# Kernel tuning notes

Measured on AMD Instinct MI355X. Metric: run time of the kernel, lower is better.

Reference implementation:

```python
import jax, jax.numpy as jnp
import numpy as np

B, T, I, H = 64, 512, 1024, 1024


def setup_inputs() -> dict:
    key = jax.random.key(0)
    k1, k2, k3, k4 = jax.random.split(key, 4)
    stdv = 1.0 / np.sqrt(H)
    x = jax.random.normal(k1, (B, T, I), dtype=jnp.float32)
    w_ih = jax.random.uniform(k2, (4 * H, I), minval=-stdv, maxval=stdv, dtype=jnp.float32)
    w_hh = jax.random.uniform(k3, (4 * H, H), minval=-stdv, maxval=stdv, dtype=jnp.float32)
    b = jax.random.uniform(k4, (4 * H,), minval=-stdv, maxval=stdv, dtype=jnp.float32)
    return {"x": x, "w_ih": w_ih, "w_hh": w_hh, "b": b}


def _lstm(x, w_ih, w_hh, b):
    # Precompute input projections for all timesteps: [T, B, 4H]
    xg = jnp.einsum('bti,gi->tbg', x, w_ih) + b

    def step(carry, xg_t):
        h, c = carry
        gates = xg_t + h @ w_hh.T  # [B, 4H]
        i, f, g, o = jnp.split(gates, 4, axis=-1)
        i = jax.nn.sigmoid(i)
        f = jax.nn.sigmoid(f)
        g = jnp.tanh(g)
        o = jax.nn.sigmoid(o)
        c = f * c + i * g
        h = o * jnp.tanh(c)
        return (h, c), (h, c)

    h0 = jnp.zeros((x.shape[0], w_hh.shape[1]), dtype=x.dtype)
    c0 = jnp.zeros_like(h0)
    _, (hs, cs) = jax.lax.scan(step, (h0, c0), xg)
    # [T, B, H] -> [B, T, H]
    return hs.transpose(1, 0, 2), cs.transpose(1, 0, 2)


def reference(x, w_ih, w_hh, b):
    return _lstm(x, w_ih, w_hh, b)
```

## Files before the change

kernel.cpp:

```cpp
#include <hip/hip_runtime.h>
#include <stdint.h>

typedef unsigned short u16;
typedef short short8 __attribute__((ext_vector_type(8)));
typedef float f32x4 __attribute__((ext_vector_type(4)));
typedef int i32x4 __attribute__((ext_vector_type(4)));
typedef unsigned long long u64;

#define NT 512
#define NH 1024
#define G4H 4096
#define HS_ELEMS 33554432ull

static __device__ __forceinline__ u16 f2bf(float f){
  union { float f; unsigned u; } v; v.f = f;
  unsigned r = v.u + 0x7fffu + ((v.u >> 16) & 1u);
  return (u16)(r >> 16);
}
static __device__ __forceinline__ float bf2f(u16 s){
  union { unsigned u; float f; } v; v.u = ((unsigned)s) << 16;
  return v.f;
}
static __device__ __forceinline__ void cvt8(const float* __restrict__ in, u16* __restrict__ out, int k){
  const float4* p = (const float4*)in;
  float4 a = p[2*k], b = p[2*k+1];
  short8 o;
  o[0]=(short)f2bf(a.x); o[1]=(short)f2bf(a.y); o[2]=(short)f2bf(a.z); o[3]=(short)f2bf(a.w);
  o[4]=(short)f2bf(b.x); o[5]=(short)f2bf(b.y); o[6]=(short)f2bf(b.z); o[7]=(short)f2bf(b.w);
  ((short8*)out)[k] = o;
}

__global__ void prep_kernel(const float* __restrict__ x,
                            const float* __restrict__ wih,
                            const float* __restrict__ whh,
                            u16* __restrict__ xb,
                            u16* __restrict__ wihb,
                            u16* __restrict__ whhb,
                            unsigned* __restrict__ hx,
                            int* __restrict__ cnt){
  int i = blockIdx.x*blockDim.x + threadIdx.x;
  int stride = gridDim.x*blockDim.x;
  for (int k = i; k < 4194304; k += stride) cvt8(x,   xb,   k);
  for (int k = i; k < 524288;  k += stride) cvt8(wih, wihb, k);
  for (int k = i; k < 524288;  k += stride) cvt8(whh, whhb, k);
  for (int k = i; k < 131072;  k += stride) hx[k] = 0u;
  if (i < 256) cnt[i] = 0;
}

__global__ __launch_bounds__(256) void gemm_xg(
    const u16* __restrict__ A,
    const u16* __restrict__ Bw,
    const float* __restrict__ bias,
    u16* __restrict__ C)
{
  __shared__ u16 lA[128*64];
  __shared__ u16 lB[128*64];
  const int tid = threadIdx.x, lane = tid & 63, w = tid >> 6;
  int bid = blockIdx.x;
  int swz = (bid & 7)*1024 + (bid >> 3);
  const int brow = swz >> 5;
  const int bcol = swz & 31;
  const int wr = (w >> 1)*64, wc = (w & 1)*64;
  f32x4 acc[4][4] = {};

  const int rA0 = brow*128 + w*32;
  const int rB0 = bcol*128 + w*32;
  for (int kt = 0; kt < 1024; kt += 64){
    const u16* gA = A  + (size_t)(rA0 + (lane>>3))*1024 + kt + (lane&7)*8;
    const u16* gB = Bw + (size_t)(rB0 + (lane>>3))*1024 + kt + (lane&7)*8;
#pragma unroll
    for (int c = 0; c < 4; c++){
      __builtin_amdgcn_global_load_lds(
        (const __attribute__((address_space(1))) void*)(gA + (size_t)c*8*1024),
        (__attribute__((address_space(3))) void*)&lA[(w*32 + c*8)*64], 16, 0, 0);
      __builtin_amdgcn_global_load_lds(
        (const __attribute__((address_space(1))) void*)(gB + (size_t)c*8*1024),
        (__attribute__((address_space(3))) void*)&lB[(w*32 + c*8)*64], 16, 0, 0);
    }
    __syncthreads();
#pragma unroll
    for (int kk = 0; kk < 2; kk++){
      short8 fa[4], fb[4];
#pragma unroll
      for (int i = 0; i < 4; i++){
        fa[i] = *(const short8*)&lA[(wr + i*16 + (lane&15))*64 + kk*32 + (lane>>4)*8];
        fb[i] = *(const short8*)&lB[(wc + i*16 + (lane&15))*64 + kk*32 + (lane>>4)*8];
      }
#pragma unroll
      for (int i = 0; i < 4; i++)
#pragma unroll
        for (int jj = 0; jj < 4; jj++)
          acc[i][jj] = __builtin_amdgcn_mfma_f32_16x16x32_bf16(fa[i], fb[jj], acc[i][jj], 0,0,0);
    }
    __syncthreads();
  }
  const int mb = brow*128 + wr + ((lane>>4)<<2);
  const int nb = bcol*128 + wc + (lane&15);
#pragma unroll
  for (int jj = 0; jj < 4; jj++){
    const int n = nb + jj*16;
    const float bv = bias[n];
#pragma unroll
    for (int i = 0; i < 4; i++){
#pragma unroll
      for (int reg = 0; reg < 4; reg++){
        int m = mb + i*16 + reg;
        C[(size_t)m*G4H + n] = f2bf(acc[i][jj][reg] + bv);
      }
    }
  }
}

__global__ __launch_bounds__(512, 2) void lstm_rec(
    const u16* __restrict__ whh,
    const u16* __restrict__ xg,
    u16* __restrict__ hx,
    int* cnt,
    float* __restrict__ hs,
    float* __restrict__ cs)
{
  __shared__ u16 lds_h[16384];
  const int tid  = threadIdx.x;
  const int lane = tid & 63;
  const int w    = tid >> 6;
  const int bid  = blockIdx.x;
  const int g    = bid >> 5;
  const int j    = bid & 31;
  const int q    = (lane & 15) >> 2;
  const int col  = j*32 + w*4 + (lane & 3);
  const int Gr   = q*1024 + col;
  const int mloc = (lane >> 4) * 4;

  i32x4 wq[32];
  {
    const i32x4* wp = (const i32x4*)(whh + (size_t)Gr*1024 + ((lane>>4)*8));
#pragma unroll
    for (int kk = 0; kk < 32; kk++) wq[kk] = wp[kk*4];
#pragma unroll
    for (int kk = 0; kk < 32; kk++) asm volatile("" : "+v"(wq[kk]));
  }

  float c_st[4] = {0.f,0.f,0.f,0.f};
  int* cntg = cnt + g*64;

  for (int t = 0; t < NT; t++){
    float xv[4];
#pragma unroll
    for (int reg = 0; reg < 4; reg++){
      int b = g*16 + mloc + reg;
      xv[reg] = bf2f(xg[((size_t)b*NT + t)*G4H + Gr]);
    }
    if (t > 0){
      if (tid == 0){
        const int need = t * 32;
        while (__hip_atomic_load(cntg, __ATOMIC_RELAXED, __HIP_MEMORY_SCOPE_AGENT) < need)
          __builtin_amdgcn_s_sleep(1);
      }
      __syncthreads();
    }
    const u64* hb64 = (const u64*)(hx + ((size_t)(((t+3)&3)*4 + g)) * 16384);
#pragma unroll
    for (int k = 0; k < 8; k++){
      int W = tid + 512*k;
      u64 v = __hip_atomic_load(hb64 + W, __ATOMIC_RELAXED, __HIP_MEMORY_SCOPE_AGENT);
      *(u64*)&lds_h[W*4] = v;
    }
    __syncthreads();

    f32x4 accv[4];
    accv[0] = (f32x4){xv[0], xv[1], xv[2], xv[3]};
    accv[1] = (f32x4){0.f,0.f,0.f,0.f};
    accv[2] = accv[1]; accv[3] = accv[1];
#pragma unroll
    for (int kk = 0; kk < 32; kk++){
      short8 av = *(const short8*)&lds_h[(kk*64 + lane)*8];
      short8 bv = __builtin_bit_cast(short8, wq[kk]);
      accv[kk & 3] = __builtin_amdgcn_mfma_f32_16x16x32_bf16(av, bv, accv[kk & 3], 0,0,0);
    }
    f32x4 gv = (accv[0] + accv[1]) + (accv[2] + accv[3]);

    u16* wbuf = hx + ((size_t)((t&3)*4 + g)) * 16384;
    float hnv[4], cnv[4];
#pragma unroll
    for (int reg = 0; reg < 4; reg++){
      float xg_ = gv[reg];
      float sig = 1.f / (1.f + __expf(-xg_));
      float th  = 1.f - 2.f / (1.f + __expf(2.f*xg_));
      float a   = (q == 2) ? th : sig;
      float v4  = __shfl_xor(a, 4);
      float v8  = __shfl_xor(a, 8);
      float v12 = __shfl_xor(a, 12);
      float iv  = (q==0)?a :(q==1)?v4:(q==2)?v8:v12;
      float fv  = (q==1)?a :(q==0)?v4:(q==3)?v8:v12;
      float gg  = (q==2)?a :(q==3)?v4:(q==0)?v8:v12;
      float ov  = (q==3)?a :(q==2)?v4:(q==1)?v8:v12;
      float cn  = fv*c_st[reg] + iv*gg;
      c_st[reg] = cn;
      float tc  = 1.f - 2.f / (1.f + __expf(2.f*cn));
      float hn  = ov * tc;
      hnv[reg] = hn; cnv[reg] = cn;
      float hp = __shfl_xor(hn, 1);
      if (q == 0 && (lane & 1) == 0){
        unsigned word = (unsigned)f2bf(hn) | ((unsigned)f2bf(hp) << 16);
        int sub = ((col & 31) >> 3)*16 + (mloc + reg);
        int idx16 = ((col >> 5)*64 + sub)*8 + (col & 7);
        __hip_atomic_store((unsigned*)(wbuf + idx16), word,
                           __ATOMIC_RELAXED, __HIP_MEMORY_SCOPE_AGENT);
      }
    }
    __syncthreads();
    if (tid == 0)
      __hip_atomic_fetch_add(cntg, 1, __ATOMIC_RELAXED, __HIP_MEMORY_SCOPE_AGENT);
#pragma unroll
    for (int reg = 0; reg < 4; reg++){
      int b = g*16 + mloc + reg;
      size_t oidx = ((size_t)b*NT + t)*NH + col;
      if (q == 1) __builtin_nontemporal_store(hnv[reg], &hs[oidx]);
      if (q == 2) __builtin_nontemporal_store(cnv[reg], &cs[oidx]);
    }
  }
}

extern "C" void kernel_launch(void* const* d_in, const int* in_sizes, int n_in,
                              void* d_out, int out_size, void* d_ws, size_t ws_size,
                              hipStream_t stream){
  const float* x    = (const float*)d_in[0];
  const float* wih  = (const float*)d_in[1];
  const float* whh  = (const float*)d_in[2];
  const float* bias = (const float*)d_in[3];
  float* hs = (float*)d_out;
  float* cs = hs + HS_ELEMS;
  char* ws = (char*)d_ws;
  u16* xg   = (u16*)(ws + 0);
  u16* xb   = (u16*)(ws + 268435456ull);
  u16* wihb = (u16*)(ws + 335544320ull);
  u16* whhb = (u16*)(ws + 343932928ull);
  u16* hx   = (u16*)(ws + 352321536ull);
  int* cnt  = (int*)(ws + 352845824ull);

  prep_kernel<<<2048, 256, 0, stream>>>(x, wih, whh, xb, wihb, whhb,
                                        (unsigned*)hx, cnt);
  gemm_xg<<<8192, 256, 0, stream>>>(xb, wihb, bias, xg);

  const u16* whhb_c = whhb; const u16* xg_c = xg;
  u16* hx_p = hx; int* cnt_p = cnt; float* hs_p = hs; float* cs_p = cs;
  void* args[6];
  args[0] = (void*)&whhb_c;
  args[1] = (void*)&xg_c;
  args[2] = (void*)&hx_p;
  args[3] = (void*)&cnt_p;
  args[4] = (void*)&hs_p;
  args[5] = (void*)&cs_p;
  hipLaunchCooperativeKernel((const void*)lstm_rec, dim3(128), dim3(512), args, 0, stream);
}
```

Baseline: 3.016 ms.

## Fuse input-projection GEMM into cooperative LSTM kernel and overlap via chunk counters

Removes the separate input-projection GEMM launch. The cooperative kernel now runs 256 blocks: 128 do the recurrence and 128 compute the xg GEMM in four time chunks of 128 steps each. Each chunk publishes completion through an atomic counter with a release fence, and the recurrence waits on that counter every 128 steps. The goal is to hide most of the GEMM behind the serial recurrence. In exchange, the GEMM gets only half the CUs, and extra LDS per block may reduce occupancy or co-residency, which a cooperative launch requires.

```diff
diff --git a/kernel.cpp b/kernel.cpp
--- a/kernel.cpp
+++ b/kernel.cpp
@@ -44,86 +44,100 @@
   for (int k = i; k < 524288;  k += stride) cvt8(wih, wihb, k);
   for (int k = i; k < 524288;  k += stride) cvt8(whh, whhb, k);
   for (int k = i; k < 131072;  k += stride) hx[k] = 0u;
-  if (i < 256) cnt[i] = 0;
-}
-
-__global__ __launch_bounds__(256) void gemm_xg(
-    const u16* __restrict__ A,
-    const u16* __restrict__ Bw,
+  if (i < 512) cnt[i] = 0;
+}
+
+__global__ __launch_bounds__(512, 2) void lstm_fused(
+    const u16* __restrict__ whh,
+    const u16* __restrict__ xb,
+    const u16* __restrict__ wihb,
     const float* __restrict__ bias,
-    u16* __restrict__ C)
-{
-  __shared__ u16 lA[128*64];
-  __shared__ u16 lB[128*64];
-  const int tid = threadIdx.x, lane = tid & 63, w = tid >> 6;
-  int bid = blockIdx.x;
-  int swz = (bid & 7)*1024 + (bid >> 3);
-  const int brow = swz >> 5;
-  const int bcol = swz & 31;
-  const int wr = (w >> 1)*64, wc = (w & 1)*64;
-  f32x4 acc[4][4] = {};
-
-  const int rA0 = brow*128 + w*32;
-  const int rB0 = bcol*128 + w*32;
-  for (int kt = 0; kt < 1024; kt += 64){
-    const u16* gA = A  + (size_t)(rA0 + (lane>>3))*1024 + kt + (lane&7)*8;
-    const u16* gB = Bw + (size_t)(rB0 + (lane>>3))*1024 + kt + (lane&7)*8;
-#pragma unroll
-    for (int c = 0; c < 4; c++){
-      __builtin_amdgcn_global_load_lds(
-        (const __attribute__((address_space(1))) void*)(gA + (size_t)c*8*1024),
-        (__attribute__((address_space(3))) void*)&lA[(w*32 + c*8)*64], 16, 0, 0);
-      __builtin_amdgcn_global_load_lds(
-        (const __attribute__((address_space(1))) void*)(gB + (size_t)c*8*1024),
-        (__attribute__((address_space(3))) void*)&lB[(w*32 + c*8)*64], 16, 0, 0);
-    }
-    __syncthreads();
-#pragma unroll
-    for (int kk = 0; kk < 2; kk++){
-      short8 fa[4], fb[4];
-#pragma unroll
-      for (int i = 0; i < 4; i++){
-        fa[i] = *(const short8*)&lA[(wr + i*16 + (lane&15))*64 + kk*32 + (lane>>4)*8];
-        fb[i] = *(const short8*)&lB[(wc + i*16 + (lane&15))*64 + kk*32 + (lane>>4)*8];
-      }
-#pragma unroll
-      for (int i = 0; i < 4; i++)
-#pragma unroll
-        for (int jj = 0; jj < 4; jj++)
-          acc[i][jj] = __builtin_amdgcn_mfma_f32_16x16x32_bf16(fa[i], fb[jj], acc[i][jj], 0,0,0);
-    }
-    __syncthreads();
-  }
-  const int mb = brow*128 + wr + ((lane>>4)<<2);
-  const int nb = bcol*128 + wc + (lane&15);
-#pragma unroll
-  for (int jj = 0; jj < 4; jj++){
-    const int n = nb + jj*16;
-    const float bv = bias[n];
-#pragma unroll
-    for (int i = 0; i < 4; i++){
-#pragma unroll
-      for (int reg = 0; reg < 4; reg++){
-        int m = mb + i*16 + reg;
-        C[(size_t)m*G4H + n] = f2bf(acc[i][jj][reg] + bv);
-      }
-    }
-  }
-}
-
-__global__ __launch_bounds__(512, 2) void lstm_rec(
-    const u16* __restrict__ whh,
-    const u16* __restrict__ xg,
+    u16* __restrict__ xg,
     u16* __restrict__ hx,
     int* cnt,
     float* __restrict__ hs,
     float* __restrict__ cs)
 {
   __shared__ u16 lds_h[16384];
+  __shared__ u16 plA[2][8192];
+  __shared__ u16 plB[2][8192];
   const int tid  = threadIdx.x;
   const int lane = tid & 63;
   const int w    = tid >> 6;
   const int bid  = blockIdx.x;
+  int* ccnt = cnt + 256;
+
+  if (bid >= 128){
+    const int pid  = bid - 128;
+    const int half = w >> 2;
+    const int w4   = w & 3;
+    const int wr   = (w4 >> 1)*64, wc = (w4 & 1)*64;
+    u16* lA = plA[half];
+    u16* lB = plB[half];
+    for (int it = 0; it < 32; ++it){
+      const int gt     = it*256 + pid*2 + half;
+      const int chunk  = gt >> 11;
+      const int within = gt & 2047;
+      const int bpan   = within >> 5;
+      const int bcol   = within & 31;
+      const int rowbase = bpan*512 + chunk*128;
+      f32x4 acc[4][4] = {};
+      const int rA0 = rowbase + w4*32;
+      const int rB0 = bcol*128 + w4*32;
+      for (int kt = 0; kt < 1024; kt += 64){
+        const u16* gA = xb   + (size_t)(rA0 + (lane>>3))*1024 + kt + (lane&7)*8;
+        const u16* gB = wihb + (size_t)(rB0 + (lane>>3))*1024 + kt + (lane&7)*8;
+#pragma unroll
+        for (int c = 0; c < 4; c++){
+          __builtin_amdgcn_global_load_lds(
+            (const __attribute__((address_space(1))) void*)(gA + (size_t)c*8*1024),
+            (__attribute__((address_space(3))) void*)&lA[(w4*32 + c*8)*64], 16, 0, 0);
+          __builtin_amdgcn_global_load_lds(
+            (const __attribute__((address_space(1))) void*)(gB + (size_t)c*8*1024),
+            (__attribute__((address_space(3))) void*)&lB[(w4*32 + c*8)*64], 16, 0, 0);
+        }
+        __syncthreads();
+#pragma unroll
+        for (int kk = 0; kk < 2; kk++){
+          short8 fa[4], fb[4];
+#pragma unroll
+          for (int i = 0; i < 4; i++){
+            fa[i] = *(const short8*)&lA[(wr + i*16 + (lane&15))*64 + kk*32 + (lane>>4)*8];
+            fb[i] = *(const short8*)&lB[(wc + i*16 + (lane&15))*64 + kk*32 + (lane>>4)*8];
+          }
+#pragma unroll
+          for (int i = 0; i < 4; i++)
+#pragma unroll
+            for (int jj = 0; jj < 4; jj++)
+              acc[i][jj] = __builtin_amdgcn_mfma_f32_16x16x32_bf16(fa[i], fb[jj], acc[i][jj], 0,0,0);
+        }
+        __syncthreads();
+      }
+      const int mb = rowbase + wr + ((lane>>4)<<2);
+      const int nb = bcol*128 + wc + (lane&15);
+#pragma unroll
+      for (int jj = 0; jj < 4; jj++){
+        const int n = nb + jj*16;
+        const float bv = bias[n];
+#pragma unroll
+        for (int i = 0; i < 4; i++){
+#pragma unroll
+          for (int reg = 0; reg < 4; reg++){
+            int m = mb + i*16 + reg;
+            xg[(size_t)m*G4H + n] = f2bf(acc[i][jj][reg] + bv);
+          }
+        }
+      }
+      __syncthreads();
+      if ((it & 7) == 7 && (tid & 255) == 0){
+        __builtin_amdgcn_fence(__ATOMIC_RELEASE, "agent");
+        __hip_atomic_fetch_add(ccnt + chunk*64, 8,
+                               __ATOMIC_RELAXED, __HIP_MEMORY_SCOPE_AGENT);
+      }
+    }
+    return;
+  }
+
   const int g    = bid >> 5;
   const int j    = bid & 31;
   const int q    = (lane & 15) >> 2;
@@ -144,6 +158,15 @@
   int* cntg = cnt + g*64;
 
   for (int t = 0; t < NT; t++){
+    if ((t & 127) == 0){
+      if (tid == 0){
+        const int k = t >> 7;
+        while (__hip_atomic_load(ccnt + k*64, __ATOMIC_RELAXED, __HIP_MEMORY_SCOPE_AGENT) < 2048)
+          __builtin_amdgcn_s_sleep(1);
+      }
+      __syncthreads();
+      __builtin_amdgcn_fence(__ATOMIC_ACQUIRE, "agent");
+    }
     float xv[4];
 #pragma unroll
     for (int reg = 0; reg < 4; reg++){
@@ -240,16 +263,20 @@
 
   prep_kernel<<<2048, 256, 0, stream>>>(x, wih, whh, xb, wihb, whhb,
                                         (unsigned*)hx, cnt);
-  gemm_xg<<<8192, 256, 0, stream>>>(xb, wihb, bias, xg);
-
-  const u16* whhb_c = whhb; const u16* xg_c = xg;
-  u16* hx_p = hx; int* cnt_p = cnt; float* hs_p = hs; float* cs_p = cs;
-  void* args[6];
+
+  const u16* whhb_c = whhb; const u16* xb_c = xb; const u16* wihb_c = wihb;
+  const float* bias_c = bias;
+  u16* xg_p = xg; u16* hx_p = hx; int* cnt_p = cnt;
+  float* hs_p = hs; float* cs_p = cs;
+  void* args[9];
   args[0] = (void*)&whhb_c;
-  args[1] = (void*)&xg_c;
-  args[2] = (void*)&hx_p;
-  args[3] = (void*)&cnt_p;
-  args[4] = (void*)&hs_p;
-  args[5] = (void*)&cs_p;
-  hipLaunchCooperativeKernel((const void*)lstm_rec, dim3(128), dim3(512), args, 0, stream);
-}
+  args[1] = (void*)&xb_c;
+  args[2] = (void*)&wihb_c;
+  args[3] = (void*)&bias_c;
+  args[4] = (void*)&xg_p;
+  args[5] = (void*)&hx_p;
+  args[6] = (void*)&cnt_p;
+  args[7] = (void*)&hs_p;
+  args[8] = (void*)&cs_p;
+  hipLaunchCooperativeKernel((const void*)lstm_fused, dim3(256), dim3(512), args, 0, stream);
+}
```

After: 2.875 ms. 1.05x faster.
